# Performance work log

Hardware: AMD Instinct MI355X
Metric: run time of the kernel (lower is better)

Reference implementation:

```python
import jax, jax.numpy as jnp
import numpy as np

B, L, DM = 2, 4096, 1024
DI = 2048      # expand * d_model
DT = 64        # dt_rank = ceil(d_model/16)
K = 4          # d_conv


def _silu(v):
    return v * jax.nn.sigmoid(v)


def setup_inputs() -> dict:
    key = jax.random.key(0)
    ks = jax.random.split(key, 9)
    s = lambda k, shape, sc: jax.random.normal(k, shape, dtype=jnp.float32) * sc
    return {
        "x": s(ks[0], (B, L, DM), 1.0),
        "in_proj_w": s(ks[1], (2 * DI, DM), 0.02),
        "conv_w": s(ks[2], (DI, 1, K), 0.1),   # depthwise: [out=DI, in/groups=1, k]
        "conv_b": s(ks[3], (DI,), 0.02),
        "x_proj_w": s(ks[4], (DT, DI), 0.02),
        "dt_proj_w": s(ks[5], (DI, DT), 0.02),
        "dt_proj_b": s(ks[6], (DI,), 0.02),
        "A_log": jax.random.uniform(ks[7], (DI,), jnp.float32, -3.0, -1.0),
        "D": jnp.ones((DI,), jnp.float32),
        "out_proj_w": s(ks[8], (DM, DI), 0.02),
    }


def reference(x, in_proj_w, conv_w, conv_b, x_proj_w, dt_proj_w, dt_proj_b,
              A_log, D, out_proj_w):
    b, l, _ = x.shape
    # input projection and gate split
    xz = jnp.einsum('bld,ed->ble', x, in_proj_w)          # [b,l,2*DI]
    xi, z = jnp.split(xz, 2, axis=-1)                     # each [b,l,DI]
    # depthwise causal conv1d (torch: padding=K-1 both sides, keep first L)
    xc = jnp.transpose(xi, (0, 2, 1))                     # [b,DI,l]
    xc = jax.lax.conv_general_dilated(
        xc, conv_w, window_strides=(1,), padding=[(K - 1, 0)],
        dimension_numbers=('NCH', 'OIH', 'NCH'),
        feature_group_count=xc.shape[1])
    xc = xc + conv_b[None, :, None]
    xi = _silu(jnp.transpose(xc, (0, 2, 1)))              # [b,l,DI]
    # dt path: x_proj -> dt_rank, dt_proj -> d_inner, softplus + clamp
    dt_low = jnp.einsum('bld,rd->blr', xi, x_proj_w)      # [b,l,DT]
    delta = jax.nn.softplus(jnp.einsum('blr,dr->bld', dt_low, dt_proj_w) + dt_proj_b)
    delta = jnp.clip(delta, 1e-6, 10.0)                   # [b,l,DI]
    A = jnp.clip(-jnp.exp(A_log), -10.0, -1e-6)           # [DI]
    e = jnp.clip(jnp.exp(delta * A), 1e-6, 1.0)           # decay factors [b,l,DI]

    # selective scan: state = clip(state*e + u)
    def step(state, eu):
        et, ut = eu
        state = jnp.clip(state * et + ut, -1e4, 1e4)
        return state, state

    init = jnp.zeros((b, xi.shape[-1]), xi.dtype)
    _, states = jax.lax.scan(step, init,
                             (jnp.swapaxes(e, 0, 1), jnp.swapaxes(xi, 0, 1)))
    y = jnp.swapaxes(states, 0, 1) + xi * D               # skip connection
    y = jnp.clip(y, -1e4, 1e4)
    y = y * _silu(z)                                      # gate
    return jnp.einsum('bld,ed->ble', y, out_proj_w)       # [b,l,DM]
```

## Files before the change

kernel.cpp:

```cpp
#include <hip/hip_runtime.h>
#include <cstdint>
#include <cstddef>

#define B_   2
#define L_   4096
#define DM_  1024
#define DI_  2048
#define DT_  64
#define M_   (B_*L_)
#define G_   64
#define CH_  (L_/G_)
#define KSPL 8
#define KSL  (DI_/KSPL)
#define BK_  32
#define LDC  136
#define LDCF 68
#define LDC3 132

typedef __bf16 bf16;
typedef __bf16 bf16x8 __attribute__((ext_vector_type(8)));
typedef __bf16 bf16x4 __attribute__((ext_vector_type(4)));
typedef float  f32x4  __attribute__((ext_vector_type(4)));

__device__ __forceinline__ float silu_f(float x){ return x / (1.f + __expf(-x)); }
__device__ __forceinline__ float softplus_f(float x){
  return fmaxf(x, 0.f) + __logf(1.f + __expf(-fabsf(x)));
}
__device__ __forceinline__ float e_of(float delta, float Ad){
  float ee = __expf(delta * Ad);
  return fminf(fmaxf(ee, 1e-6f), 1.f);
}
__device__ __forceinline__ float a_of(const float* alog, int d){
  float Ad = -__expf(alog[d]);
  return fminf(fmaxf(Ad, -10.f), -1e-6f);
}

__device__ __forceinline__ void gl_lds16(const bf16* g, bf16* l){
  __builtin_amdgcn_global_load_lds(
      (const __attribute__((address_space(1))) void*)g,
      (__attribute__((address_space(3))) void*)l, 16, 0, 0);
}

__device__ __forceinline__ void ds_read128(bf16x8& d, uint32_t addr){
  asm volatile("ds_read_b128 %0, %1" : "=v"(d) : "v"(addr));
}

__global__ __launch_bounds__(256)
void cvt_all_kernel(const float4* __restrict__ s0, bf16x4* __restrict__ d0, int n0,
                    const float4* __restrict__ s1, bf16x4* __restrict__ d1, int n1,
                    const float4* __restrict__ s2, bf16x4* __restrict__ d2, int n2,
                    const float4* __restrict__ s3, bf16x4* __restrict__ d3, int n3,
                    const float4* __restrict__ s4, bf16x4* __restrict__ d4, int n4)
{
  int i = blockIdx.x*256 + threadIdx.x;
  const float4* s; bf16x4* d;
  if      (i < n0)                 { s = s0; d = d0; }
  else if ((i -= n0) < n1)         { s = s1; d = d1; }
  else if ((i -= n1) < n2)         { s = s2; d = d2; }
  else if ((i -= n2) < n3)         { s = s3; d = d3; }
  else if ((i -= n3) < n4)         { s = s4; d = d4; }
  else return;
  float4 v = s[i];
  bf16x4 o = {(bf16)v.x, (bf16)v.y, (bf16)v.z, (bf16)v.w};
  d[i] = o;
}

template<int OUT, int MT, int NT, int KT>
__global__ __launch_bounds__(512, 2)
void gemm256(const bf16* __restrict__ A, const bf16* __restrict__ W,
             bf16* __restrict__ ob, bf16* __restrict__ ob2,
             float* __restrict__ of)
{
  __shared__ __align__(16) char smem[131072];
  char* lA = smem;
  char* lB = smem + 65536;

  const int t    = threadIdx.x;
  const int lane = t & 63;
  const int wave = t >> 6;
  const int wm   = wave >> 2;
  const int wn   = wave & 3;
  const int l16  = lane & 15, quad = lane >> 4;

  const int nnt = NT / 256;
  const int nwg = (MT/256) * nnt;
  const int cpx = nwg >> 3;
  int lin = (blockIdx.x & 7) * cpx + (blockIdx.x >> 3);
  const int m0 = (lin / nnt) * 256;
  const int n0 = (lin % nnt) * 256;

  const int r8     = lane >> 3;
  const int lchunk = (lane & 7) ^ r8;
  const bf16* ap[4]; const bf16* bp[4];
  #pragma unroll
  for (int s = 0; s < 4; ++s){
    ap[s] = A + (size_t)(m0 + s*64 + wave*8 + r8) * KT + lchunk*8;
    bp[s] = W + (size_t)(n0 + s*64 + wave*8 + r8) * KT + lchunk*8;
  }

  const uint32_t lAu = (uint32_t)(uintptr_t)(__attribute__((address_space(3))) char*)lA;
  const uint32_t lBu = (uint32_t)(uintptr_t)(__attribute__((address_space(3))) char*)lB;
  const uint32_t swz0 = (uint32_t)(((quad    ) ^ (l16 & 7)) << 4);
  const uint32_t swz1 = (uint32_t)(((4 | quad) ^ (l16 & 7)) << 4);
  const uint32_t aB0 = lAu + (uint32_t)((wm*128 + l16) * 128) + swz0;
  const uint32_t aB1 = lAu + (uint32_t)((wm*128 + l16) * 128) + swz1;
  const uint32_t bB0 = lBu + (uint32_t)((wn*64  + l16) * 128) + swz0;
  const uint32_t bB1 = lBu + (uint32_t)((wn*64  + l16) * 128) + swz1;

  f32x4 acc[8][4] = {};
  constexpr int NTILES = KT / 64;

  gl_lds16(bp[0], (bf16*)(lB + 0*8192 + wave*1024)); bp[0] += 64;
  gl_lds16(bp[1], (bf16*)(lB + 1*8192 + wave*1024)); bp[1] += 64;
  gl_lds16(bp[2], (bf16*)(lB + 2*8192 + wave*1024)); bp[2] += 64;
  gl_lds16(bp[3], (bf16*)(lB + 3*8192 + wave*1024)); bp[3] += 64;
  gl_lds16(ap[0], (bf16*)(lA + 0*8192 + wave*1024)); ap[0] += 64;
  gl_lds16(ap[2], (bf16*)(lA + 2*8192 + wave*1024)); ap[2] += 64;
  gl_lds16(ap[1], (bf16*)(lA + 1*8192 + wave*1024)); ap[1] += 64;
  gl_lds16(ap[3], (bf16*)(lA + 3*8192 + wave*1024)); ap[3] += 64;
  asm volatile("s_waitcnt vmcnt(2)" ::: "memory");
  __builtin_amdgcn_s_barrier();

  for (int tt = 0; tt < NTILES; ++tt){
    const int u = tt & 1;
    const uint32_t ub = (uint32_t)(u << 15);
    char* sA = lA + (u^1)*32768;
    char* sB = lB + (u^1)*32768;
    const bool notlast = (tt + 1 < NTILES);

    bf16x8 a0k0[4], a0k1[4], b0k0[2], b0k1[2];
    #pragma unroll
    for (int mi = 0; mi < 4; ++mi) ds_read128(a0k0[mi], aB0 + ub + mi*2048);
    #pragma unroll
    for (int mi = 0; mi < 4; ++mi) ds_read128(a0k1[mi], aB1 + ub + mi*2048);
    #pragma unroll
    for (int ni = 0; ni < 2; ++ni) ds_read128(b0k0[ni], bB0 + ub + ni*2048);
    #pragma unroll
    for (int ni = 0; ni < 2; ++ni) ds_read128(b0k1[ni], bB1 + ub + ni*2048);
    if (notlast){
      gl_lds16(bp[0], (bf16*)(sB + 0*8192 + wave*1024)); bp[0] += 64;
      gl_lds16(bp[1], (bf16*)(sB + 1*8192 + wave*1024)); bp[1] += 64;
    }
    asm volatile("s_waitcnt lgkmcnt(8)" ::: "memory");
    __builtin_amdgcn_s_barrier();
    asm volatile("s_waitcnt lgkmcnt(0)" ::: "memory");
    __builtin_amdgcn_sched_barrier(0);
    __builtin_amdgcn_s_setprio(1);
    #pragma unroll
    for (int mi = 0; mi < 4; ++mi)
      #pragma unroll
      for (int ni = 0; ni < 2; ++ni)
        acc[mi][ni] = __builtin_amdgcn_mfma_f32_16x16x32_bf16(a0k0[mi], b0k0[ni], acc[mi][ni], 0, 0, 0);
    #pragma unroll
    for (int mi = 0; mi < 4; ++mi)
      #pragma unroll
      for (int ni = 0; ni < 2; ++ni)
        acc[mi][ni] = __builtin_amdgcn_mfma_f32_16x16x32_bf16(a0k1[mi], b0k1[ni], acc[mi][ni], 0, 0, 0);
    __builtin_amdgcn_s_setprio(0);
    __builtin_amdgcn_sched_barrier(0);
    __builtin_amdgcn_s_barrier();

    bf16x8 b1k0[2], b1k1[2];
    #pragma unroll
    for (int ni = 0; ni < 2; ++ni) ds_read128(b1k0[ni], bB0 + ub + (2+ni)*2048);
    #pragma unroll
    for (int ni = 0; ni < 2; ++ni) ds_read128(b1k1[ni], bB1 + ub + (2+ni)*2048);
    if (notlast){
      gl_lds16(bp[2], (bf16*)(sB + 2*8192 + wave*1024)); bp[2] += 64;
      gl_lds16(bp[3], (bf16*)(sB + 3*8192 + wave*1024)); bp[3] += 64;
    }
    __builtin_amdgcn_s_barrier();
    asm volatile("s_waitcnt lgkmcnt(0)" ::: "memory");
    __builtin_amdgcn_sched_barrier(0);
    __builtin_amdgcn_s_setprio(1);
    #pragma unroll
    for (int mi = 0; mi < 4; ++mi)
      #pragma unroll
      for (int ni = 0; ni < 2; ++ni)
        acc[mi][2+ni] = __builtin_amdgcn_mfma_f32_16x16x32_bf16(a0k0[mi], b1k0[ni], acc[mi][2+ni], 0, 0, 0);
    #pragma unroll
    for (int mi = 0; mi < 4; ++mi)
      #pragma unroll
      for (int ni = 0; ni < 2; ++ni)
        acc[mi][2+ni] = __builtin_amdgcn_mfma_f32_16x16x32_bf16(a0k1[mi], b1k1[ni], acc[mi][2+ni], 0, 0, 0);
    __builtin_amdgcn_s_setprio(0);
    __builtin_amdgcn_sched_barrier(0);
    if (notlast) asm volatile("s_waitcnt vmcnt(4)" ::: "memory");
    else         asm volatile("s_waitcnt vmcnt(0)" ::: "memory");
    __builtin_amdgcn_s_barrier();

    bf16x8 a1k0[4], a1k1[4];
    #pragma unroll
    for (int mi = 0; mi < 4; ++mi) ds_read128(a1k0[mi], aB0 + ub + (4+mi)*2048);
    #pragma unroll
    for (int mi = 0; mi < 4; ++mi) ds_read128(a1k1[mi], aB1 + ub + (4+mi)*2048);
    if (notlast){
      gl_lds16(ap[0], (bf16*)(sA + 0*8192 + wave*1024)); ap[0] += 64;
      gl_lds16(ap[2], (bf16*)(sA + 2*8192 + wave*1024)); ap[2] += 64;
    }
    __builtin_amdgcn_s_barrier();
    asm volatile("s_waitcnt lgkmcnt(0)" ::: "memory");
    __builtin_amdgcn_sched_barrier(0);
    __builtin_amdgcn_s_setprio(1);
    #pragma unroll
    for (int mi = 0; mi < 4; ++mi)
      #pragma unroll
      for (int ni = 0; ni < 2; ++ni)
        acc[4+mi][2+ni] = __builtin_amdgcn_mfma_f32_16x16x32_bf16(a1k0[mi], b1k0[ni], acc[4+mi][2+ni], 0, 0, 0);
    #pragma unroll
    for (int mi = 0; mi < 4; ++mi)
      #pragma unroll
      for (int ni = 0; ni < 2; ++ni)
        acc[4+mi][2+ni] = __builtin_amdgcn_mfma_f32_16x16x32_bf16(a1k1[mi], b1k1[ni], acc[4+mi][2+ni], 0, 0, 0);
    __builtin_amdgcn_s_setprio(0);
    __builtin_amdgcn_sched_barrier(0);
    __builtin_amdgcn_s_barrier();

    if (notlast){
      gl_lds16(ap[1], (bf16*)(sA + 1*8192 + wave*1024)); ap[1] += 64;
      gl_lds16(ap[3], (bf16*)(sA + 3*8192 + wave*1024)); ap[3] += 64;
    }
    __builtin_amdgcn_s_barrier();
    __builtin_amdgcn_sched_barrier(0);
    __builtin_amdgcn_s_setprio(1);
    #pragma unroll
    for (int mi = 0; mi < 4; ++mi)
      #pragma unroll
      for (int ni = 0; ni < 2; ++ni)
        acc[4+mi][ni] = __builtin_amdgcn_mfma_f32_16x16x32_bf16(a1k0[mi], b0k0[ni], acc[4+mi][ni], 0, 0, 0);
    #pragma unroll
    for (int mi = 0; mi < 4; ++mi)
      #pragma unroll
      for (int ni = 0; ni < 2; ++ni)
        acc[4+mi][ni] = __builtin_amdgcn_mfma_f32_16x16x32_bf16(a1k1[mi], b0k1[ni], acc[4+mi][ni], 0, 0, 0);
    __builtin_amdgcn_s_setprio(0);
    __builtin_amdgcn_sched_barrier(0);
    if (notlast) asm volatile("s_waitcnt vmcnt(2)" ::: "memory");
    __builtin_amdgcn_s_barrier();
  }

  if (OUT == 3){
    float* Cf = (float*)smem;
    #pragma unroll
    for (int pass = 0; pass < 4; ++pass){
      if (wm == (pass >> 1)){
        #pragma unroll
        for (int mi2 = 0; mi2 < 4; ++mi2){
          const int mi = (pass & 1)*4 + mi2;
          #pragma unroll
          for (int ni = 0; ni < 4; ++ni)
            #pragma unroll
            for (int r = 0; r < 4; ++r)
              Cf[(mi2*16 + quad*4 + r)*264 + wn*64 + ni*16 + l16] = acc[mi][ni][r];
        }
      }
      __syncthreads();
      #pragma unroll
      for (int it = 0; it < 8; ++it){
        const int row = it*8 + (t >> 6);
        const int c4  = (t & 63) * 4;
        float4 v = *(const float4*)&Cf[row*264 + c4];
        *(float4*)&of[(size_t)(m0 + pass*64 + row)*NT + n0 + c4] = v;
      }
      __syncthreads();
    }
  } else {
    bf16* Cs = (bf16*)smem;
    const bool isg  = (n0 >= DI_);
    bf16* outp      = isg ? ob2 : ob;
    const int ncol0 = isg ? (n0 - DI_) : n0;
    #pragma unroll
    for (int pass = 0; pass < 2; ++pass){
      if (wm == pass){
        #pragma unroll
        for (int mi = 0; mi < 8; ++mi)
          #pragma unroll
          for (int ni = 0; ni < 4; ++ni)
            #pragma unroll
            for (int r = 0; r < 4; ++r){
              float v = acc[mi][ni][r];
              if (isg) v = silu_f(v);
              Cs[(mi*16 + quad*4 + r)*264 + wn*64 + ni*16 + l16] = (bf16)v;
            }
      }
      __syncthreads();
      #pragma unroll
      for (int it = 0; it < 8; ++it){
        const int row = it*16 + (t >> 5);
        const int c8  = (t & 31) * 8;
        bf16x8 v = *(const bf16x8*)&Cs[row*264 + c8];
        *(bf16x8*)&outp[(size_t)(m0 + pass*128 + row)*DI_ + ncol0 + c8] = v;
      }
      __syncthreads();
    }
  }
}

template<int EPI, int MT, int NT, int KT>
__global__ __launch_bounds__(256)
void gemm_bt(const bf16* __restrict__ A, const bf16* __restrict__ W,
             float* __restrict__ o0, bf16* __restrict__ ob, bf16* __restrict__ ob2,
             const float* __restrict__ bias, const float* __restrict__ alog,
             const bf16* __restrict__ uq, float* __restrict__ Pq,
             float* __restrict__ Fq)
{
  __shared__ char smem[34816];
  bf16* As = (bf16*)smem;
  bf16* Bs = (bf16*)(smem + 128*BK_*2);
  const int t    = threadIdx.x;
  const int lane = t & 63;
  const int wave = t >> 6;
  const int wm   = wave >> 1, wn = wave & 1;
  const int l16  = lane & 15, quad = lane >> 4;

  int m0, n0;
  if (EPI == 4){
    m0 = blockIdx.y * 128; n0 = 0;
  } else {
    const int gx  = NT / 128;
    const int lin = blockIdx.y * gx + blockIdx.x;
    const int grp = lin / (gx * 4);
    const int rem = lin % (gx * 4);
    m0 = (grp * 4 + (rem & 3)) * 128;
    n0 = (rem >> 2) * 128;
  }

  const int srow = (lane >> 2);
  const int scol = (lane & 3) * 8;

  const int KFULL = (EPI == 4) ? (KT * KSPL) : KT;
  const int kbase = (EPI == 4) ? (int)blockIdx.z * KT : 0;

  const int rowA0 = m0 + wave*32 + srow;
  int rB0 = n0 + wave*32 + srow, rB1 = rB0 + 16;
  if (NT < 128){ rB0 = (rB0 >= NT) ? NT-1 : rB0; rB1 = (rB1 >= NT) ? NT-1 : rB1; }
  const bf16* ap0 = A + (size_t)rowA0*KFULL        + kbase + scol;
  const bf16* ap1 = A + (size_t)(rowA0+16)*KFULL   + kbase + scol;
  const bf16* bp0 = W + (size_t)rB0*KFULL          + kbase + scol;
  const bf16* bp1 = W + (size_t)rB1*KFULL          + kbase + scol;
  bf16* lA0 = &As[(wave*32)*BK_];
  bf16* lA1 = &As[(wave*32+16)*BK_];
  bf16* lB0 = &Bs[(wave*32)*BK_];
  bf16* lB1 = &Bs[(wave*32+16)*BK_];

  f32x4 acc[4][4] = {};
  constexpr int kframes = KT / BK_;

  for (int kt = 0; kt < kframes; ++kt){
    gl_lds16(ap0, lA0);  gl_lds16(ap1, lA1);
    gl_lds16(bp0, lB0);  gl_lds16(bp1, lB1);
    ap0 += BK_; ap1 += BK_; bp0 += BK_; bp1 += BK_;
    __syncthreads();
    bf16x8 af[4], bf_[4];
    #pragma unroll
    for (int i = 0; i < 4; ++i){
      af[i]  = *(const bf16x8*)&As[(wm*64 + i*16 + l16)*BK_ + quad*8];
      bf_[i] = *(const bf16x8*)&Bs[(wn*64 + i*16 + l16)*BK_ + quad*8];
    }
    #pragma unroll
    for (int mi = 0; mi < 4; ++mi)
      #pragma unroll
      for (int ni = 0; ni < 4; ++ni)
        acc[mi][ni] = __builtin_amdgcn_mfma_f32_16x16x32_bf16(af[mi], bf_[ni], acc[mi][ni], 0, 0, 0);
    __syncthreads();
  }

  if (EPI == 4){
    float* Cf = (float*)smem;
    if (wn == 0){
      #pragma unroll
      for (int mi = 0; mi < 4; ++mi)
        #pragma unroll
        for (int ni = 0; ni < 4; ++ni)
          #pragma unroll
          for (int r = 0; r < 4; ++r)
            Cf[(wm*64 + mi*16 + quad*4 + r)*LDCF + ni*16 + l16] = acc[mi][ni][r];
    }
    __syncthreads();
    #pragma unroll
    for (int it = 0; it < 8; ++it){
      const int row = it*16 + (t >> 4);
      const int c4  = (t & 15) * 4;
      float4 v = *(const float4*)&Cf[row*LDCF + c4];
      *(float4*)&o0[((size_t)blockIdx.z*M_ + m0 + row)*DT_ + c4] = v;
    }
  } else {
    bf16* Cs = (bf16*)smem;
    #pragma unroll
    for (int mi = 0; mi < 4; ++mi){
      #pragma unroll
      for (int ni = 0; ni < 4; ++ni){
        const int n = n0 + wn*64 + ni*16 + l16;
        #pragma unroll
        for (int r = 0; r < 4; ++r){
          float v = acc[mi][ni][r];
          v = softplus_f(v + bias[n]);
          v = fminf(fmaxf(v, 1e-6f), 10.f);
          Cs[(wm*64 + mi*16 + quad*4 + r)*LDC + wn*64 + ni*16 + l16] = (bf16)v;
        }
      }
    }
    __syncthreads();
    #pragma unroll
    for (int it = 0; it < 8; ++it){
      const int row = it*16 + (t >> 4);
      const int c8  = (t & 15) * 8;
      bf16x8 v = *(const bf16x8*)&Cs[row*LDC + c8];
      *(bf16x8*)&ob[(size_t)(m0+row)*NT + n0 + c8] = v;
    }
    {
      const int chunk = t >> 7;
      const int dcol  = t & 127;
      const int dglob = n0 + dcol;
      const float Ad  = a_of(alog, dglob);
      const int b  = m0 >> 12;
      const int c0 = (m0 & 4095) >> 6;
      const size_t ubase = (size_t)(m0 + chunk*64)*DI_ + dglob;
      float p = 1.f, f = 0.f;
      for (int i = 0; i < CH_; ++i){
        float dl = (float)Cs[(chunk*64 + i)*LDC + dcol];
        float ee = e_of(dl, Ad);
        float uu = (float)uq[ubase + (size_t)i*DI_];
        f = f*ee + uu;
        p *= ee;
      }
      const size_t o = ((size_t)(b*G_ + c0 + chunk))*DI_ + dglob;
      Pq[o] = p; Fq[o] = f;
    }
  }
}

__global__ __launch_bounds__(256)
void dt_reduce_kernel(const float* __restrict__ part, bf16* __restrict__ dtl){
  const int i = blockIdx.x*256 + threadIdx.x;
  float s = 0.f;
  #pragma unroll
  for (int z = 0; z < KSPL; ++z) s += part[(size_t)z*M_*DT_ + i];
  dtl[i] = (bf16)s;
}

__global__ __launch_bounds__(256)
void conv_silu_kernel(const bf16* __restrict__ xi, const float* __restrict__ cw,
                      const float* __restrict__ cb, bf16* __restrict__ ubf)
{
  const int idx = blockIdx.x*256 + threadIdx.x;
  const int d = idx & (DI_-1);
  const int l = (idx >> 11) & (L_-1);
  float s = cb[d];
  #pragma unroll
  for (int k = 0; k < 4; ++k){
    const int ll = l + k - 3;
    if (ll >= 0) s += (float)xi[idx + (k-3)*DI_] * cw[d*4 + k];
  }
  ubf[idx] = (bf16)silu_f(s);
}

__global__ __launch_bounds__(256)
void scan_pass3(const bf16* __restrict__ delta, const bf16* __restrict__ u,
                const bf16* __restrict__ g, const float* __restrict__ P,
                const float* __restrict__ F, const float* __restrict__ alog,
                const float* __restrict__ Dp, bf16* __restrict__ y)
{
  const int d = blockIdx.x*256 + threadIdx.x;
  const int c = blockIdx.y, b = blockIdx.z;
  const float Ad = a_of(alog, d);
  float s = 0.f;
  for (int cc = 0; cc < c; ++cc){
    const size_t o = ((size_t)(b*G_ + cc))*DI_ + d;
    s = F[o] + P[o]*s;
  }
  size_t base = ((size_t)(b*L_ + c*CH_))*DI_ + d;
  const float Dd = Dp[d];
  for (int i = 0; i < CH_; ++i){
    const size_t idx = base + (size_t)i*DI_;
    const float uu = (float)u[idx];
    s = s*e_of((float)delta[idx], Ad) + uu;
    float yy = s + uu*Dd;
    yy = fminf(fmaxf(yy, -1e4f), 1e4f);
    yy *= (float)g[idx];
    y[idx] = (bf16)yy;
  }
}

extern "C" void kernel_launch(void* const* d_in, const int* in_sizes, int n_in,
                              void* d_out, int out_size, void* d_ws, size_t ws_size,
                              hipStream_t stream)
{
  (void)in_sizes; (void)n_in; (void)out_size; (void)ws_size;
  const float* x        = (const float*)d_in[0];
  const float* in_w     = (const float*)d_in[1];
  const float* conv_w   = (const float*)d_in[2];
  const float* conv_b   = (const float*)d_in[3];
  const float* xproj_w  = (const float*)d_in[4];
  const float* dtproj_w = (const float*)d_in[5];
  const float* dtproj_b = (const float*)d_in[6];
  const float* A_log    = (const float*)d_in[7];
  const float* Dp       = (const float*)d_in[8];
  const float* out_w    = (const float*)d_in[9];

  char* base = (char*)d_ws;
  const size_t MiB = 1024*1024;
  bf16*  xi_bf = (bf16*) (base + 0);
  float* part  = (float*)(base + 0);
  bf16*  dl_bf = (bf16*) (base + 0);
  bf16*  x_bf  = (bf16*) (base + 32*MiB);
  bf16*  w1_bf = (bf16*) (base + 48*MiB);
  bf16*  g_bf  = (bf16*) (base + 64*MiB);
  bf16*  u_bf  = (bf16*) (base + 96*MiB);
  bf16*  y_bf  = (bf16*) (base + 128*MiB);
  bf16*  wo_bf = (bf16*) (base + 160*MiB);
  bf16*  xp_bf = (bf16*) (base + 164*MiB);
  bf16*  dp_bf = (bf16*) (base + 165*MiB);
  bf16*  dtl_bf= (bf16*) (base + 166*MiB);
  float* P     = (float*)(base + 167*MiB);
  float* F     = (float*)(base + 168*MiB);

  const int c0 = (M_*DM_)/4, c1 = (2*DI_*DM_)/4, c2 = (DT_*DI_)/4,
            c3 = (DI_*DT_)/4, c4 = (DM_*DI_)/4;
  const int ctot = c0+c1+c2+c3+c4;
  cvt_all_kernel<<<(ctot+255)/256, 256, 0, stream>>>(
      (const float4*)x,        (bf16x4*)x_bf,  c0,
      (const float4*)in_w,     (bf16x4*)w1_bf, c1,
      (const float4*)xproj_w,  (bf16x4*)xp_bf, c2,
      (const float4*)dtproj_w, (bf16x4*)dp_bf, c3,
      (const float4*)out_w,    (bf16x4*)wo_bf, c4);

  gemm256<0, M_, 2*DI_, DM_><<<dim3((M_/256)*((2*DI_)/256)), 512, 0, stream>>>(
      x_bf, w1_bf, xi_bf, g_bf, nullptr);
  conv_silu_kernel<<<(M_*DI_)/256, 256, 0, stream>>>(xi_bf, conv_w, conv_b, u_bf);
  gemm_bt<4, M_, DT_, KSL><<<dim3(1, M_/128, KSPL), 256, 0, stream>>>(
      u_bf, xp_bf, part, nullptr, nullptr, nullptr,
      nullptr, nullptr, nullptr, nullptr);
  dt_reduce_kernel<<<(M_*DT_)/256, 256, 0, stream>>>(part, dtl_bf);
  gemm_bt<2, M_, DI_, DT_><<<dim3(DI_/128, M_/128), 256, 0, stream>>>(
      dtl_bf, dp_bf, nullptr, dl_bf, nullptr, dtproj_b,
      A_log, u_bf, P, F);
  scan_pass3<<<dim3(DI_/256, G_, B_), 256, 0, stream>>>(
      dl_bf, u_bf, g_bf, P, F, A_log, Dp, y_bf);
  gemm256<3, M_, DM_, DI_><<<dim3((M_/256)*(DM_/256)), 512, 0, stream>>>(
      y_bf, wo_bf, nullptr, nullptr, (float*)d_out);
}
```

Before: 404.5 us.

## Specialize out-proj GEMM to 256x128 tiles and vectorize conv and dt-reduce kernels

Splits the templated GEMM into an in-proj variant and a dedicated out-proj variant. The out-proj variant uses 256x128 output tiles, which doubles the workgroup count from 128 to 256 so more CUs are busy on the M=8192, N=1024 problem. The conv+SiLU kernel now handles 8 channels per thread with 16-byte bf16 loads and float4 weight loads. The dt partial-sum reduce now processes 4 floats per thread. Smaller out-proj tiles mean less operand reuse per workgroup and a tighter memory-to-MFMA ratio.

```diff
diff --git a/kernel.cpp b/kernel.cpp
--- a/kernel.cpp
+++ b/kernel.cpp
@@ -15,7 +15,6 @@
 #define BK_  32
 #define LDC  136
 #define LDCF 68
-#define LDC3 132
 
 typedef __bf16 bf16;
 typedef __bf16 bf16x8 __attribute__((ext_vector_type(8)));
@@ -65,12 +64,13 @@
   d[i] = o;
 }
 
-template<int OUT, int MT, int NT, int KT>
 __global__ __launch_bounds__(512, 2)
-void gemm256(const bf16* __restrict__ A, const bf16* __restrict__ W,
-             bf16* __restrict__ ob, bf16* __restrict__ ob2,
-             float* __restrict__ of)
+void gemm256_xz(const bf16* __restrict__ A, const bf16* __restrict__ W,
+                bf16* __restrict__ ob, bf16* __restrict__ ob2)
 {
+  constexpr int MT = M_;
+  constexpr int NT = 2*DI_;
+  constexpr int KT = DM_;
   __shared__ __align__(16) char smem[131072];
   char* lA = smem;
   char* lB = smem + 65536;
@@ -239,60 +239,210 @@
     __builtin_amdgcn_s_barrier();
   }
 
-  if (OUT == 3){
-    float* Cf = (float*)smem;
-    #pragma unroll
-    for (int pass = 0; pass < 4; ++pass){
-      if (wm == (pass >> 1)){
+  bf16* Cs = (bf16*)smem;
+  const bool isg  = (n0 >= DI_);
+  bf16* outp      = isg ? ob2 : ob;
+  const int ncol0 = isg ? (n0 - DI_) : n0;
+  #pragma unroll
+  for (int pass = 0; pass < 2; ++pass){
+    if (wm == pass){
+      #pragma unroll
+      for (int mi = 0; mi < 8; ++mi)
         #pragma unroll
-        for (int mi2 = 0; mi2 < 4; ++mi2){
-          const int mi = (pass & 1)*4 + mi2;
+        for (int ni = 0; ni < 4; ++ni)
           #pragma unroll
-          for (int ni = 0; ni < 4; ++ni)
-            #pragma unroll
-            for (int r = 0; r < 4; ++r)
-              Cf[(mi2*16 + quad*4 + r)*264 + wn*64 + ni*16 + l16] = acc[mi][ni][r];
-        }
+          for (int r = 0; r < 4; ++r){
+            float v = acc[mi][ni][r];
+            if (isg) v = silu_f(v);
+            Cs[(mi*16 + quad*4 + r)*264 + wn*64 + ni*16 + l16] = (bf16)v;
+          }
+    }
+    __syncthreads();
+    #pragma unroll
+    for (int it = 0; it < 8; ++it){
+      const int row = it*16 + (t >> 5);
+      const int c8  = (t & 31) * 8;
+      bf16x8 v = *(const bf16x8*)&Cs[row*264 + c8];
+      *(bf16x8*)&outp[(size_t)(m0 + pass*128 + row)*DI_ + ncol0 + c8] = v;
+    }
+    __syncthreads();
+  }
+}
+
+__global__ __launch_bounds__(512, 2)
+void gemm256_out(const bf16* __restrict__ A, const bf16* __restrict__ W,
+                 float* __restrict__ of)
+{
+  constexpr int MT = M_;
+  constexpr int NT = DM_;
+  constexpr int KT = DI_;
+  __shared__ __align__(16) char smem[131072];
+  char* lA = smem;
+  char* lB = smem + 65536;
+
+  const int t    = threadIdx.x;
+  const int lane = t & 63;
+  const int wave = t >> 6;
+  const int wm   = wave >> 2;
+  const int wn   = wave & 3;
+  const int l16  = lane & 15, quad = lane >> 4;
+
+  const int nnt = NT / 128;
+  const int nwg = (MT/256) * nnt;
+  const int cpx = nwg >> 3;
+  int lin = (blockIdx.x & 7) * cpx + (blockIdx.x >> 3);
+  const int m0 = (lin / nnt) * 256;
+  const int n0 = (lin % nnt) * 128;
+
+  const int r8     = lane >> 3;
+  const int lchunk = (lane & 7) ^ r8;
+  const bf16* ap[4]; const bf16* bp[2];
+  #pragma unroll
+  for (int s = 0; s < 4; ++s)
+    ap[s] = A + (size_t)(m0 + s*64 + wave*8 + r8) * KT + lchunk*8;
+  #pragma unroll
+  for (int s = 0; s < 2; ++s)
+    bp[s] = W + (size_t)(n0 + s*64 + wave*8 + r8) * KT + lchunk*8;
+
+  const uint32_t lAu = (uint32_t)(uintptr_t)(__attribute__((address_space(3))) char*)lA;
+  const uint32_t lBu = (uint32_t)(uintptr_t)(__attribute__((address_space(3))) char*)lB;
+  const uint32_t swz0 = (uint32_t)(((quad    ) ^ (l16 & 7)) << 4);
+  const uint32_t swz1 = (uint32_t)(((4 | quad) ^ (l16 & 7)) << 4);
+  const uint32_t aB0 = lAu + (uint32_t)((wm*128 + l16) * 128) + swz0;
+  const uint32_t aB1 = lAu + (uint32_t)((wm*128 + l16) * 128) + swz1;
+  const uint32_t bB0 = lBu + (uint32_t)((wn*32 + l16) * 128) + swz0;
+  const uint32_t bB1 = lBu + (uint32_t)((wn*32 + l16) * 128) + swz1;
+
+  f32x4 acc[8][2] = {};
+  constexpr int NTILES = KT / 64;
+
+  gl_lds16(bp[0], (bf16*)(lB + 0*8192 + wave*1024)); bp[0] += 64;
+  gl_lds16(bp[1], (bf16*)(lB + 1*8192 + wave*1024)); bp[1] += 64;
+  gl_lds16(ap[0], (bf16*)(lA + 0*8192 + wave*1024)); ap[0] += 64;
+  gl_lds16(ap[2], (bf16*)(lA + 2*8192 + wave*1024)); ap[2] += 64;
+  gl_lds16(ap[1], (bf16*)(lA + 1*8192 + wave*1024)); ap[1] += 64;
+  gl_lds16(ap[3], (bf16*)(lA + 3*8192 + wave*1024)); ap[3] += 64;
+  asm volatile("s_waitcnt vmcnt(2)" ::: "memory");
+  __builtin_amdgcn_s_barrier();
+
+  for (int tt = 0; tt < NTILES; ++tt){
+    const int u = tt & 1;
+    const uint32_t ub = (uint32_t)(u << 15);
+    char* sA = lA + (u^1)*32768;
+    char* sB = lB + (u^1)*32768;
+    const bool notlast = (tt + 1 < NTILES);
+
+    bf16x8 a0k0[4], a0k1[4], b0k0[1], b0k1[1];
+    #pragma unroll
+    for (int mi = 0; mi < 4; ++mi) ds_read128(a0k0[mi], aB0 + ub + mi*2048);
+    #pragma unroll
+    for (int mi = 0; mi < 4; ++mi) ds_read128(a0k1[mi], aB1 + ub + mi*2048);
+    ds_read128(b0k0[0], bB0 + ub);
+    ds_read128(b0k1[0], bB1 + ub);
+    if (notlast){
+      gl_lds16(bp[0], (bf16*)(sB + 0*8192 + wave*1024)); bp[0] += 64;
+      gl_lds16(bp[1], (bf16*)(sB + 1*8192 + wave*1024)); bp[1] += 64;
+    }
+    __builtin_amdgcn_s_barrier();
+    asm volatile("s_waitcnt lgkmcnt(0)" ::: "memory");
+    __builtin_amdgcn_sched_barrier(0);
+    __builtin_amdgcn_s_setprio(1);
+    #pragma unroll
+    for (int mi = 0; mi < 4; ++mi)
+      acc[mi][0] = __builtin_amdgcn_mfma_f32_16x16x32_bf16(a0k0[mi], b0k0[0], acc[mi][0], 0, 0, 0);
+    #pragma unroll
+    for (int mi = 0; mi < 4; ++mi)
+      acc[mi][0] = __builtin_amdgcn_mfma_f32_16x16x32_bf16(a0k1[mi], b0k1[0], acc[mi][0], 0, 0, 0);
+    __builtin_amdgcn_s_setprio(0);
+    __builtin_amdgcn_sched_barrier(0);
+    __builtin_amdgcn_s_barrier();
+
+    bf16x8 b1k0[1], b1k1[1];
+    ds_read128(b1k0[0], bB0 + ub + 2048);
+    ds_read128(b1k1[0], bB1 + ub + 2048);
+    if (notlast){
+      gl_lds16(ap[0], (bf16*)(sA + 0*8192 + wave*1024)); ap[0] += 64;
+    }
+    __builtin_amdgcn_s_barrier();
+    asm volatile("s_waitcnt lgkmcnt(0)" ::: "memory");
+    __builtin_amdgcn_sched_barrier(0);
+    __builtin_amdgcn_s_setprio(1);
+    #pragma unroll
+    for (int mi = 0; mi < 4; ++mi)
+      acc[mi][1] = __builtin_amdgcn_mfma_f32_16x16x32_bf16(a0k0[mi], b1k0[0], acc[mi][1], 0, 0, 0);
+    #pragma unroll
+    for (int mi = 0; mi < 4; ++mi)
+      acc[mi][1] = __builtin_amdgcn_mfma_f32_16x16x32_bf16(a0k1[mi], b1k1[0], acc[mi][1], 0, 0, 0);
+    __builtin_amdgcn_s_setprio(0);
+    __builtin_amdgcn_sched_barrier(0);
+    if (notlast) asm volatile("s_waitcnt vmcnt(3)" ::: "memory");
+    else         asm volatile("s_waitcnt vmcnt(0)" ::: "memory");
+    __builtin_amdgcn_s_barrier();
+
+    bf16x8 a1k0[4], a1k1[4];
+    #pragma unroll
+    for (int mi = 0; mi < 4; ++mi) ds_read128(a1k0[mi], aB0 + ub + (4+mi)*2048);
+    #pragma unroll
+    for (int mi = 0; mi < 4; ++mi) ds_read128(a1k1[mi], aB1 + ub + (4+mi)*2048);
+    if (notlast){
+      gl_lds16(ap[2], (bf16*)(sA + 2*8192 + wave*1024)); ap[2] += 64;
+      gl_lds16(ap[1], (bf16*)(sA + 1*8192 + wave*1024)); ap[1] += 64;
+    }
+    __builtin_amdgcn_s_barrier();
+    asm volatile("s_waitcnt lgkmcnt(0)" ::: "memory");
+    __builtin_amdgcn_sched_barrier(0);
+    __builtin_amdgcn_s_setprio(1);
+    #pragma unroll
+    for (int mi = 0; mi < 4; ++mi)
+      acc[4+mi][1] = __builtin_amdgcn_mfma_f32_16x16x32_bf16(a1k0[mi], b1k0[0], acc[4+mi][1], 0, 0, 0);
+    #pragma unroll
+    for (int mi = 0; mi < 4; ++mi)
+      acc[4+mi][1] = __builtin_amdgcn_mfma_f32_16x16x32_bf16(a1k1[mi], b1k1[0], acc[4+mi][1], 0, 0, 0);
+    __builtin_amdgcn_s_setprio(0);
+    __builtin_amdgcn_sched_barrier(0);
+    __builtin_amdgcn_s_barrier();
+
+    if (notlast){
+      gl_lds16(ap[3], (bf16*)(sA + 3*8192 + wave*1024)); ap[3] += 64;
+    }
+    __builtin_amdgcn_s_barrier();
+    __builtin_amdgcn_sched_barrier(0);
+    __builtin_amdgcn_s_setprio(1);
+    #pragma unroll
+    for (int mi = 0; mi < 4; ++mi)
+      acc[4+mi][0] = __builtin_amdgcn_mfma_f32_16x16x32_bf16(a1k0[mi], b0k0[0], acc[4+mi][0], 0, 0, 0);
+    #pragma unroll
+    for (int mi = 0; mi < 4; ++mi)
+      acc[4+mi][0] = __builtin_amdgcn_mfma_f32_16x16x32_bf16(a1k1[mi], b0k1[0], acc[4+mi][0], 0, 0, 0);
+    __builtin_amdgcn_s_setprio(0);
+    __builtin_amdgcn_sched_barrier(0);
+    if (notlast) asm volatile("s_waitcnt vmcnt(2)" ::: "memory");
+    __builtin_amdgcn_s_barrier();
+  }
+
+  float* Cf = (float*)smem;
+  #pragma unroll
+  for (int pass = 0; pass < 4; ++pass){
+    if (wm == (pass >> 1)){
+      #pragma unroll
+      for (int mi2 = 0; mi2 < 4; ++mi2){
+        const int mi = (pass & 1)*4 + mi2;
+        #pragma unroll
+        for (int ni = 0; ni < 2; ++ni)
+          #pragma unroll
+          for (int r = 0; r < 4; ++r)
+            Cf[(mi2*16 + quad*4 + r)*132 + wn*32 + ni*16 + l16] = acc[mi][ni][r];
       }
-      __syncthreads();
-      #pragma unroll
-      for (int it = 0; it < 8; ++it){
-        const int row = it*8 + (t >> 6);
-        const int c4  = (t & 63) * 4;
-        float4 v = *(const float4*)&Cf[row*264 + c4];
-        *(float4*)&of[(size_t)(m0 + pass*64 + row)*NT + n0 + c4] = v;
-      }
-      __syncthreads();
-    }
-  } else {
-    bf16* Cs = (bf16*)smem;
-    const bool isg  = (n0 >= DI_);
-    bf16* outp      = isg ? ob2 : ob;
-    const int ncol0 = isg ? (n0 - DI_) : n0;
-    #pragma unroll
-    for (int pass = 0; pass < 2; ++pass){
-      if (wm == pass){
-        #pragma unroll
-        for (int mi = 0; mi < 8; ++mi)
-          #pragma unroll
-          for (int ni = 0; ni < 4; ++ni)
-            #pragma unroll
-            for (int r = 0; r < 4; ++r){
-              float v = acc[mi][ni][r];
-              if (isg) v = silu_f(v);
-              Cs[(mi*16 + quad*4 + r)*264 + wn*64 + ni*16 + l16] = (bf16)v;
-            }
-      }
-      __syncthreads();
-      #pragma unroll
-      for (int it = 0; it < 8; ++it){
-        const int row = it*16 + (t >> 5);
-        const int c8  = (t & 31) * 8;
-        bf16x8 v = *(const bf16x8*)&Cs[row*264 + c8];
-        *(bf16x8*)&outp[(size_t)(m0 + pass*128 + row)*DI_ + ncol0 + c8] = v;
-      }
-      __syncthreads();
-    }
+    }
+    __syncthreads();
+    #pragma unroll
+    for (int it = 0; it < 4; ++it){
+      const int row = it*16 + (t >> 5);
+      const int c4  = (t & 31) * 4;
+      float4 v = *(const float4*)&Cf[row*132 + c4];
+      *(float4*)&of[(size_t)(m0 + pass*64 + row)*NT + n0 + c4] = v;
+    }
+    __syncthreads();
   }
 }
 
@@ -432,27 +582,47 @@
 
 __global__ __launch_bounds__(256)
 void dt_reduce_kernel(const float* __restrict__ part, bf16* __restrict__ dtl){
-  const int i = blockIdx.x*256 + threadIdx.x;
-  float s = 0.f;
-  #pragma unroll
-  for (int z = 0; z < KSPL; ++z) s += part[(size_t)z*M_*DT_ + i];
-  dtl[i] = (bf16)s;
+  const int i = (blockIdx.x*256 + threadIdx.x) * 4;
+  float4 s = *(const float4*)&part[i];
+  #pragma unroll
+  for (int z = 1; z < KSPL; ++z){
+    float4 v = *(const float4*)&part[(size_t)z*M_*DT_ + i];
+    s.x += v.x; s.y += v.y; s.z += v.z; s.w += v.w;
+  }
+  bf16x4 o = {(bf16)s.x, (bf16)s.y, (bf16)s.z, (bf16)s.w};
+  *(bf16x4*)&dtl[i] = o;
 }
 
 __global__ __launch_bounds__(256)
 void conv_silu_kernel(const bf16* __restrict__ xi, const float* __restrict__ cw,
                       const float* __restrict__ cb, bf16* __restrict__ ubf)
 {
-  const int idx = blockIdx.x*256 + threadIdx.x;
-  const int d = idx & (DI_-1);
-  const int l = (idx >> 11) & (L_-1);
-  float s = cb[d];
+  const int row = blockIdx.x;
+  const int l   = row & (L_-1);
+  const int d0  = threadIdx.x * 8;
+  const size_t base = (size_t)row*DI_ + d0;
+  float s[8];
+  #pragma unroll
+  for (int j = 0; j < 8; ++j) s[j] = cb[d0+j];
+  float w[8][4];
+  #pragma unroll
+  for (int j = 0; j < 8; ++j){
+    float4 wv = *(const float4*)&cw[(d0+j)*4];
+    w[j][0] = wv.x; w[j][1] = wv.y; w[j][2] = wv.z; w[j][3] = wv.w;
+  }
   #pragma unroll
   for (int k = 0; k < 4; ++k){
     const int ll = l + k - 3;
-    if (ll >= 0) s += (float)xi[idx + (k-3)*DI_] * cw[d*4 + k];
-  }
-  ubf[idx] = (bf16)silu_f(s);
+    if (ll >= 0){
+      bf16x8 xv = *(const bf16x8*)&xi[base + (ptrdiff_t)(k-3)*DI_];
+      #pragma unroll
+      for (int j = 0; j < 8; ++j) s[j] += (float)xv[j] * w[j][k];
+    }
+  }
+  bf16x8 o;
+  #pragma unroll
+  for (int j = 0; j < 8; ++j) o[j] = (bf16)silu_f(s[j]);
+  *(bf16x8*)&ubf[base] = o;
 }
 
 __global__ __launch_bounds__(256)
@@ -525,18 +695,16 @@
       (const float4*)dtproj_w, (bf16x4*)dp_bf, c3,
       (const float4*)out_w,    (bf16x4*)wo_bf, c4);
 
-  gemm256<0, M_, 2*DI_, DM_><<<dim3((M_/256)*((2*DI_)/256)), 512, 0, stream>>>(
-      x_bf, w1_bf, xi_bf, g_bf, nullptr);
-  conv_silu_kernel<<<(M_*DI_)/256, 256, 0, stream>>>(xi_bf, conv_w, conv_b, u_bf);
+  gemm256_xz<<<dim3(512), 512, 0, stream>>>(x_bf, w1_bf, xi_bf, g_bf);
+  conv_silu_kernel<<<M_, 256, 0, stream>>>(xi_bf, conv_w, conv_b, u_bf);
   gemm_bt<4, M_, DT_, KSL><<<dim3(1, M_/128, KSPL), 256, 0, stream>>>(
       u_bf, xp_bf, part, nullptr, nullptr, nullptr,
       nullptr, nullptr, nullptr, nullptr);
-  dt_reduce_kernel<<<(M_*DT_)/256, 256, 0, stream>>>(part, dtl_bf);
+  dt_reduce_kernel<<<(M_*DT_)/1024, 256, 0, stream>>>(part, dtl_bf);
   gemm_bt<2, M_, DI_, DT_><<<dim3(DI_/128, M_/128), 256, 0, stream>>>(
       dtl_bf, dp_bf, nullptr, dl_bf, nullptr, dtproj_b,
       A_log, u_bf, P, F);
   scan_pass3<<<dim3(DI_/256, G_, B_), 256, 0, stream>>>(
       dl_bf, u_bf, g_bf, P, F, A_log, Dp, y_bf);
-  gemm256<3, M_, DM_, DI_><<<dim3((M_/256)*(DM_/256)), 512, 0, stream>>>(
-      y_bf, wo_bf, nullptr, nullptr, (float*)d_out);
-}
+  gemm256_out<<<dim3(256), 512, 0, stream>>>(y_bf, wo_bf, (float*)d_out);
+}
```

Measured after the change: 377.3 us. -6.7%, faster.
